# Optimization experiments

Measured on AMD Instinct MI355X. Metric: run time of the kernel, lower is better.

## Reference

```python
import math
import jax, jax.numpy as jnp
import numpy as np

D_MODEL = 256
NUM_HEAD = 8
NUM_LEVEL = 1
KERNEL = 5
NUM_POINT = KERNEL * KERNEL
NUM_VAR = 5  # with_rotation=True
HEAD_DIM = D_MODEL // NUM_HEAD


def _kernel_indices(k=KERNEL):
    # odd kernel: linspace(-(k-1)/2, (k-1)/2, k); torch.meshgrid default 'ij'; stack([j,i])/k
    idx = jnp.linspace(-(k - 1) / 2.0, (k - 1) / 2.0, k)
    ii, jj = jnp.meshgrid(idx, idx, indexing='ij')
    return jnp.stack([jj, ii], axis=-1).reshape(-1, 2) / k  # (P, 2)


def setup_inputs() -> dict:
    key = jax.random.key(0)
    ks = jax.random.split(key, 8)
    B, LQ = 2, 4096
    Hf, Wf = 188, 188
    LV = Hf * Wf
    d = D_MODEL
    nb = NUM_LEVEL * NUM_HEAD * NUM_VAR
    na = NUM_HEAD * NUM_LEVEL * NUM_POINT
    return {
        'query': jax.random.normal(ks[0], (B, LQ, d), jnp.float32),
        'value': jax.random.normal(ks[1], (B, LV, d), jnp.float32),
        'ref_windows': jax.random.uniform(ks[2], (B, LQ, 7), jnp.float32),
        'W_box': jax.random.normal(ks[3], (nb, d), jnp.float32) * 0.02,
        'b_box': jax.random.uniform(ks[4], (nb,), jnp.float32),
        'W_attn': jax.random.normal(ks[5], (na, d), jnp.float32) * 0.02,
        'b_attn': jnp.zeros((na,), jnp.float32),
        'W_value': jax.random.normal(ks[6], (d, d), jnp.float32) * 0.02,
        'b_value': jnp.zeros((d,), jnp.float32),
        'W_out': jax.random.normal(ks[7], (d, d), jnp.float32) * 0.02,
        'b_out': jnp.zeros((d,), jnp.float32),
        'H_feat': Hf,
        'W_feat': Wf,
    }


def reference(query, value, ref_windows, W_box, b_box, W_attn, b_attn,
              W_value, b_value, W_out, b_out, H_feat, W_feat):
    B, LQ, d = query.shape
    LV = value.shape[1]
    Hh, Lv, P, Dh = NUM_HEAD, NUM_LEVEL, NUM_POINT, HEAD_DIM

    # value projection -> (B, LV, Hh, Dh)
    v = (value @ W_value.T + b_value).reshape(B, LV, Hh, Dh)

    # attention weights: softmax over (level*point) per head
    attn = jax.nn.softmax((query @ W_attn.T + b_attn).reshape(B, LQ, Hh, Lv * P), axis=-1)
    attn = attn.reshape(B, LQ, Hh, Lv, P)

    # --- _where_to_attend ---
    ob = (query @ W_box.T + b_box).reshape(B, LQ, Hh, Lv, NUM_VAR)
    rw = ref_windows[:, :, None, None, :]                    # (B,LQ,1,1,7)
    ref_boxes = rw[..., jnp.array([0, 1, 3, 4])]             # cx, cy, w, h
    ref_angles = rw[..., 6:7]
    off_boxes, off_angles = ob[..., :4], ob[..., 4:5]
    angles = (ref_angles + off_angles / 16.0) * (2.0 * math.pi)
    boxes = ref_boxes + off_boxes / 8.0 * ref_boxes[..., jnp.array([2, 3, 2, 3])]
    center = boxes[..., None, :2]                            # (B,LQ,Hh,Lv,1,2)
    size = boxes[..., None, 2:4]
    cos_a, sin_a = jnp.cos(angles), jnp.sin(angles)
    rot = jnp.stack([cos_a, -sin_a, sin_a, cos_a], axis=-1).reshape(B, LQ, Hh, Lv, 1, 2, 2)
    g = _kernel_indices() * jax.nn.relu(size)                # (B,LQ,Hh,Lv,P,2)
    grid = center + (g[..., None, :] * rot).sum(-1)          # (B,LQ,Hh,Lv,P,2), normalized [0,1]

    # --- single-level bilinear sampling (align_corners=False, zero padding) ---
    gl = grid[:, :, :, 0]                                    # (B,LQ,Hh,P,2)
    gx = gl[..., 0] * W_feat - 0.5
    gy = gl[..., 1] * H_feat - 0.5
    x0 = jnp.floor(gx)
    y0 = jnp.floor(gy)
    x0i = x0.astype(jnp.int32)
    y0i = y0.astype(jnp.int32)
    wx1 = gx - x0
    wy1 = gy - y0
    wx0 = 1.0 - wx1
    wy0 = 1.0 - wy1

    b_idx = jnp.arange(B)[:, None, None, None]
    h_idx = jnp.arange(Hh)[None, None, :, None]

    def gather(yi, xi):
        valid = (xi >= 0) & (xi < W_feat) & (yi >= 0) & (yi < H_feat)
        lin = jnp.clip(yi, 0, H_feat - 1) * W_feat + jnp.clip(xi, 0, W_feat - 1)
        return v[b_idx, lin, h_idx] * valid[..., None]       # (B,LQ,Hh,P,Dh)

    s = (gather(y0i, x0i) * (wy0 * wx0)[..., None]
         + gather(y0i, x0i + 1) * (wy0 * wx1)[..., None]
         + gather(y0i + 1, x0i) * (wy1 * wx0)[..., None]
         + gather(y0i + 1, x0i + 1) * (wy1 * wx1)[..., None])

    out_heads = (s * attn[:, :, :, 0, :, None]).sum(axis=3)  # (B,LQ,Hh,Dh)
    out = out_heads.reshape(B, LQ, Hh * Dh) @ W_out.T + b_out
    attn_w = attn.reshape(B, LQ, Hh, Lv, KERNEL, KERNEL)
    return out, attn_w
```

## Files before the change

### kernel.cpp

```cpp
#include <hip/hip_runtime.h>


typedef float floatx4 __attribute__((ext_vector_type(4)));
typedef short shortx8 __attribute__((ext_vector_type(8)));

static __device__ __forceinline__ unsigned short f2bf(float x) {
    unsigned int u = __float_as_uint(x);
    return (unsigned short)((u + 0x7fffu + ((u >> 16) & 1u)) >> 16);
}
static __device__ __forceinline__ unsigned int pack2(float a, float b) {
    return (unsigned int)f2bf(a) | ((unsigned int)f2bf(b) << 16);
}
static __device__ __forceinline__ void async16(const void* g, void* lds) {
    __builtin_amdgcn_global_load_lds(
        (const __attribute__((address_space(1))) unsigned int*)g,
        (__attribute__((address_space(3))) unsigned int*)lds, 16, 0, 0);
}

__global__ __launch_bounds__(256) void convert_kernel(
    const float* __restrict__ value, unsigned short* __restrict__ vbf, long long nv4,
    const float* __restrict__ W_value, unsigned short* __restrict__ wvbf,
    const float* __restrict__ W_attn, const float* __restrict__ W_box,
    unsigned short* __restrict__ wabf, float* __restrict__ Wab,
    const float* __restrict__ W_out, unsigned short* __restrict__ wobf,
    const float* __restrict__ b_attn, const float* __restrict__ b_box,
    float* __restrict__ bab)
{
    const int NBV = 2048;
    const int blk = blockIdx.x, tid = threadIdx.x;
    if (blk < NBV) {
        for (long long i = (long long)blk * 256 + tid; i < nv4; i += (long long)NBV * 256) {
            float4 f = ((const float4*)value)[i];
            ((uint2*)vbf)[i] = make_uint2(pack2(f.x, f.y), pack2(f.z, f.w));
        }
    } else if (blk < NBV + 16) {
        int base = (blk - NBV) * 1024 + tid;
#pragma unroll
        for (int k = 0; k < 4; ++k) {
            int j = base + k * 256;
            float4 f = ((const float4*)W_value)[j];
            ((uint2*)wvbf)[j] = make_uint2(pack2(f.x, f.y), pack2(f.z, f.w));
        }
    } else if (blk < NBV + 32) {
        int base = (blk - NBV - 16) * 1024 + tid;
#pragma unroll
        for (int k = 0; k < 4; ++k) {
            int j = base + k * 256;
            int row = j >> 6, col = (j & 63) * 4;
            float4 f;
            if (row < 200)      f = *(const float4*)(W_attn + (size_t)row * 256 + col);
            else if (row < 240) f = *(const float4*)(W_box + (size_t)(row - 200) * 256 + col);
            else                f = make_float4(0.f, 0.f, 0.f, 0.f);
            ((uint2*)wabf)[j] = make_uint2(pack2(f.x, f.y), pack2(f.z, f.w));
            ((float4*)Wab)[j] = f;
        }
    } else if (blk < NBV + 48) {
        int base = (blk - NBV - 32) * 1024 + tid;
#pragma unroll
        for (int k = 0; k < 4; ++k) {
            int j = base + k * 256;
            float4 f = ((const float4*)W_out)[j];
            ((uint2*)wobf)[j] = make_uint2(pack2(f.x, f.y), pack2(f.z, f.w));
        }
    } else {
        bab[tid] = tid < 200 ? b_attn[tid] : (tid < 240 ? b_box[tid - 200] : 0.f);
    }
}

template <int OUTMODE>
__global__ __launch_bounds__(256) void gemm_bf16(
    const unsigned short* __restrict__ A,
    const unsigned short* __restrict__ Bw,
    const float* __restrict__ bias,
    void* __restrict__ Cv, int M, int LV)
{
    __shared__ unsigned short As[128 * 64];
    __shared__ unsigned short Bs[128 * 64];
    const int tid = threadIdx.x;
    const int wv = tid >> 6, lane = tid & 63;
    const int lr = lane & 15, lq = lane >> 4;
    const int m0 = blockIdx.x * 128, n0 = blockIdx.y * 128;
    const int wm = wv & 1, wn = wv >> 1;
    const int srow = tid >> 3;
    const int scol = (tid & 7) * 8;

    floatx4 acc[4][4];
#pragma unroll
    for (int i = 0; i < 4; ++i)
#pragma unroll
        for (int j = 0; j < 4; ++j) acc[i][j] = (floatx4){0.f, 0.f, 0.f, 0.f};

    for (int kc = 0; kc < 4; ++kc) {
        const int k0 = kc * 64;
        __syncthreads();
#pragma unroll
        for (int i = 0; i < 4; ++i) {
            int ra = m0 + i * 32 + srow; ra = ra < M ? ra : M - 1;
            async16(A + (size_t)ra * 256 + k0 + scol, (char*)As + i * 4096 + wv * 1024);
            int rb = n0 + i * 32 + srow;
            async16(Bw + (size_t)rb * 256 + k0 + scol, (char*)Bs + i * 4096 + wv * 1024);
        }
        __syncthreads();
#pragma unroll
        for (int kk = 0; kk < 64; kk += 32) {
            shortx8 af[4], bfr[4];
#pragma unroll
            for (int t = 0; t < 4; ++t) {
                af[t]  = *(const shortx8*)&As[(wm * 64 + t * 16 + lr) * 64 + kk + lq * 8];
                bfr[t] = *(const shortx8*)&Bs[(wn * 64 + t * 16 + lr) * 64 + kk + lq * 8];
            }
#pragma unroll
            for (int ti = 0; ti < 4; ++ti)
#pragma unroll
                for (int tj = 0; tj < 4; ++tj)
                    acc[ti][tj] = __builtin_amdgcn_mfma_f32_16x16x32_bf16(bfr[tj], af[ti], acc[ti][tj], 0, 0, 0);
        }
    }
#pragma unroll
    for (int ti = 0; ti < 4; ++ti) {
        int m = m0 + wm * 64 + ti * 16 + lr;
        if (m >= M) continue;
        if (OUTMODE == 0) {
            float* Crow = (float*)Cv + (size_t)m * 256;
#pragma unroll
            for (int tj = 0; tj < 4; ++tj) {
                int nb = n0 + wn * 64 + tj * 16 + lq * 4;
                float4 bv = *(const float4*)(bias + nb);
                float4 o = make_float4(acc[ti][tj][0] + bv.x, acc[ti][tj][1] + bv.y,
                                       acc[ti][tj][2] + bv.z, acc[ti][tj][3] + bv.w);
                *(float4*)(Crow + nb) = o;
            }
        } else {
            int b = m >= LV ? 1 : 0;
            int lv = m - (b ? LV : 0);
#pragma unroll
            for (int tj = 0; tj < 4; ++tj) {
                int nb = n0 + wn * 64 + tj * 16 + lq * 4;
                float4 bv = *(const float4*)(bias + nb);
                int h = nb >> 5, dh = nb & 31;
                unsigned short* dst = (unsigned short*)Cv + ((size_t)(b * 8 + h) * LV + lv) * 32 + dh;
                *(uint2*)dst = make_uint2(pack2(acc[ti][tj][0] + bv.x, acc[ti][tj][1] + bv.y),
                                          pack2(acc[ti][tj][2] + bv.z, acc[ti][tj][3] + bv.w));
            }
        }
    }
}

__global__ __launch_bounds__(256) void gemm_nt_bias(
    const float* __restrict__ A, const float* __restrict__ W,
    const float* __restrict__ bias, float* __restrict__ C, int M)
{
    const int K = 256, N = 256;
    __shared__ float As[16][68];
    __shared__ float Bs[16][68];
    int tid = threadIdx.x;
    int tcol = tid & 15, trow = tid >> 4;
    int m0 = blockIdx.x * 64, n0 = blockIdx.y * 64;
    int lr = tid >> 2, lc = (tid & 3) << 2;
    float acc[4][4] = {};
    for (int k0 = 0; k0 < K; k0 += 16) {
        int arow = m0 + lr; if (arow > M - 1) arow = M - 1;
        float4 av = *(const float4*)(A + (size_t)arow * K + k0 + lc);
        float4 wv = *(const float4*)(W + (size_t)(n0 + lr) * K + k0 + lc);
        __syncthreads();
        As[lc + 0][lr] = av.x; As[lc + 1][lr] = av.y; As[lc + 2][lr] = av.z; As[lc + 3][lr] = av.w;
        Bs[lc + 0][lr] = wv.x; Bs[lc + 1][lr] = wv.y; Bs[lc + 2][lr] = wv.z; Bs[lc + 3][lr] = wv.w;
        __syncthreads();
#pragma unroll
        for (int k = 0; k < 16; ++k) {
            float4 a4 = *(const float4*)&As[k][trow << 2];
            float4 b4 = *(const float4*)&Bs[k][tcol << 2];
            float a[4] = {a4.x, a4.y, a4.z, a4.w};
            float bb[4] = {b4.x, b4.y, b4.z, b4.w};
#pragma unroll
            for (int i = 0; i < 4; i++)
#pragma unroll
                for (int j = 0; j < 4; j++) acc[i][j] += a[i] * bb[j];
        }
    }
#pragma unroll
    for (int i = 0; i < 4; i++) {
        int m = m0 + trow * 4 + i;
        if (m >= M) continue;
#pragma unroll
        for (int j = 0; j < 4; j++) {
            int n = n0 + tcol * 4 + j;
            C[(size_t)m * N + n] = acc[i][j] + bias[n];
        }
    }
}

__global__ __launch_bounds__(256) void decode_sample_kernel(
    const unsigned short* __restrict__ v,
    const float* __restrict__ logits,
    const float* __restrict__ ref_windows,
    float* __restrict__ attn_out,
    unsigned short* __restrict__ ohbf,
    const int* __restrict__ Hf_p, const int* __restrict__ Wf_p, int LV, int LQ)
{
    __shared__ float lg[8][32];
    __shared__ float rw[8][7];
    __shared__ float prm[8][6];
    __shared__ float mxinv[8][2];
    __shared__ uint4 pk[8][25][2];

    const int s = blockIdx.x, c = blockIdx.y;
    const int b = s >> 3, h = s & 7;
    const int tid = threadIdx.x;
    const int Hf = *Hf_p, Wf = *Wf_p;
    const size_t mbase = (size_t)b * LQ + c * 8;

    if (tid < 240) {
        int qq = tid / 30, j = tid - qq * 30;
        int col = (j < 25) ? h * 25 + j : 200 + h * 5 + (j - 25);
        lg[qq][j] = logits[(mbase + qq) * 256 + col];
    }
    if (tid < 56) {
        int qq = tid / 7, k = tid - qq * 7;
        rw[qq][k] = ref_windows[(mbase + qq) * 7 + k];
    }
    __syncthreads();

    if (tid < 8) {
        int qq = tid;
        float mx = -1e30f;
#pragma unroll
        for (int p = 0; p < 25; p++) mx = fmaxf(mx, lg[qq][p]);
        float ssum = 0.f;
#pragma unroll
        for (int p = 0; p < 25; p++) ssum += expf(lg[qq][p] - mx);
        mxinv[qq][0] = mx; mxinv[qq][1] = 1.f / ssum;
        float cx = rw[qq][0] + lg[qq][25] * 0.125f * rw[qq][3];
        float cy = rw[qq][1] + lg[qq][26] * 0.125f * rw[qq][4];
        float bw = rw[qq][3] + lg[qq][27] * 0.125f * rw[qq][3];
        float bh = rw[qq][4] + lg[qq][28] * 0.125f * rw[qq][4];
        float ang = (rw[qq][6] + lg[qq][29] * 0.0625f) * 6.283185307179586f;
        prm[qq][0] = cx; prm[qq][1] = cy;
        prm[qq][2] = fmaxf(bw, 0.f); prm[qq][3] = fmaxf(bh, 0.f);
        prm[qq][4] = cosf(ang); prm[qq][5] = sinf(ang);
    }
    __syncthreads();

    if (tid < 200) {
        int qq = tid / 25, p = tid - qq * 25;
        float a = expf(lg[qq][p] - mxinv[qq][0]) * mxinv[qq][1];
        attn_out[(mbase + qq) * 200 + h * 25 + p] = a;
        int pi = p / 5, pj = p - pi * 5;
        float g0 = (float)(pj - 2) * 0.2f * prm[qq][2];
        float g1 = (float)(pi - 2) * 0.2f * prm[qq][3];
        float ca = prm[qq][4], sa = prm[qq][5];
        float gx = (prm[qq][0] + g0 * ca - g1 * sa) * (float)Wf - 0.5f;
        float gy = (prm[qq][1] + g0 * sa + g1 * ca) * (float)Hf - 0.5f;
        float x0f = floorf(gx), y0f = floorf(gy);
        int x0 = (int)x0f, y0 = (int)y0f;
        float wx1 = gx - x0f, wy1 = gy - y0f;
        float wx0 = 1.f - wx1, wy0 = 1.f - wy1;
        int y1 = y0 + 1;
        int bx; float wl, wr;
        if (x0 >= 0 && x0 <= Wf - 2)      { bx = x0;     wl = wx0; wr = wx1; }
        else if (x0 == -1)                { bx = 0;      wl = wx1; wr = 0.f; }
        else if (x0 == Wf - 1)            { bx = Wf - 2; wl = 0.f; wr = wx0; }
        else                              { bx = 0;      wl = 0.f; wr = 0.f; }
        float wy0v = (y0 >= 0 && y0 < Hf) ? wy0 : 0.f;
        float wy1v = (y1 >= 0 && y1 < Hf) ? wy1 : 0.f;
        int cy0 = min(max(y0, 0), Hf - 1), cy1 = min(max(y1, 0), Hf - 1);
        unsigned off0 = (unsigned)(cy0 * Wf + bx) * 16u;
        unsigned off1 = (unsigned)(cy1 * Wf + bx) * 16u;
        float aw0 = a * wy0v, aw1 = a * wy1v;
        pk[qq][p][0] = make_uint4(__float_as_uint(aw0 * wl), __float_as_uint(aw1 * wl), off0, off1);
        pk[qq][p][1] = make_uint4(__float_as_uint(aw0 * wr), __float_as_uint(aw1 * wr), off0, off1);
    }
    __syncthreads();

    const int qq = tid >> 5, l = tid & 31;
    const unsigned int* vw = (const unsigned int*)(v + (size_t)s * LV * 32);
    const uint4* pkp = &pk[qq][0][l >> 4];
    float e0 = 0.f, o0 = 0.f, e1 = 0.f, o1 = 0.f;
#pragma unroll
    for (int p = 0; p < 25; ++p) {
        uint4 t = pkp[2 * p];
        float w0 = __uint_as_float(t.x), w1 = __uint_as_float(t.y);
        unsigned u0 = vw[t.z + l];
        unsigned u1 = vw[t.w + l];
        e0 += w0 * __uint_as_float(u0 << 16);
        o0 += w0 * __uint_as_float(u0 & 0xffff0000u);
        e1 += w1 * __uint_as_float(u1 << 16);
        o1 += w1 * __uint_as_float(u1 & 0xffff0000u);
    }
    float a0 = e0 + e1, a1 = o0 + o1;
    a0 += __shfl_xor(a0, 16, 32);
    a1 += __shfl_xor(a1, 16, 32);
    if (l < 16)
        ((unsigned int*)ohbf)[(mbase + qq) * 128 + h * 16 + l] = pack2(a0, a1);
}

extern "C" void kernel_launch(void* const* d_in, const int* in_sizes, int n_in,
                              void* d_out, int out_size, void* d_ws, size_t ws_size,
                              hipStream_t stream) {
    const float* query       = (const float*)d_in[0];
    const float* value       = (const float*)d_in[1];
    const float* ref_windows = (const float*)d_in[2];
    const float* W_box       = (const float*)d_in[3];
    const float* b_box       = (const float*)d_in[4];
    const float* W_attn      = (const float*)d_in[5];
    const float* b_attn      = (const float*)d_in[6];
    const float* W_value     = (const float*)d_in[7];
    const float* b_value     = (const float*)d_in[8];
    const float* W_out       = (const float*)d_in[9];
    const float* b_out       = (const float*)d_in[10];
    const int*   Hf          = (const int*)d_in[11];
    const int*   Wf          = (const int*)d_in[12];

    const int M1 = in_sizes[1] / 256;
    const int MQ = in_sizes[0] / 256;
    const int LQ = MQ / 2;
    const int LV = M1 / 2;

    unsigned short* vbf  = (unsigned short*)d_ws;
    unsigned short* Vout = vbf + (size_t)M1 * 256;
    unsigned short* ohbf = Vout + (size_t)M1 * 256;
    unsigned short* wvbf = ohbf + (size_t)MQ * 256;
    unsigned short* wabf = wvbf + 65536;
    unsigned short* wobf = wabf + 65536;
    float* Wab       = (float*)(wobf + 65536);
    float* bab       = Wab + 65536;
    float* logits    = bab + 256;

    float* out0     = (float*)d_out;
    float* attn_out = out0 + (size_t)MQ * 256;

    const long long nv4 = (long long)M1 * 64;

    convert_kernel<<<2097, 256, 0, stream>>>(value, vbf, nv4, W_value, wvbf,
                                             W_attn, W_box, wabf, Wab,
                                             W_out, wobf, b_attn, b_box, bab);
    dim3 g1((M1 + 127) / 128, 2);
    gemm_bf16<1><<<g1, 256, 0, stream>>>(vbf, wvbf, b_value, Vout, M1, LV);
    dim3 g2(MQ / 64, 4);
    gemm_nt_bias<<<g2, 256, 0, stream>>>(query, Wab, bab, logits, MQ);
    decode_sample_kernel<<<dim3(16, LQ / 8), 256, 0, stream>>>(
        Vout, logits, ref_windows, attn_out, ohbf, Hf, Wf, LV, LQ);
    dim3 g4(MQ / 128, 2);
    gemm_bf16<0><<<g4, 256, 0, stream>>>(ohbf, wobf, b_out, out0, MQ, LV);
}
```

Baseline: 220.3 us.

## Fuse value fp32-to-bf16 conversion into projection GEMM and retile output GEMM

The separate pass that converted the large value tensor to bf16 is removed. The value-projection GEMM now reads fp32 rows directly, converts them in registers and stores bf16 into shared memory, which avoids a full write and reread of the converted tensor. The output GEMM uses 64-row tiles to launch more blocks, and the decode/sample kernel remaps block indices so consecutive blocks cover the same (batch, head) slices, for better cache locality. The cost is that the fused A loads are synchronous and no longer async-to-LDS, so they may stall the GEMM's load phase.

```diff
diff --git a/kernel.cpp b/kernel.cpp
--- a/kernel.cpp
+++ b/kernel.cpp
@@ -18,31 +18,24 @@
 }
 
 __global__ __launch_bounds__(256) void convert_kernel(
-    const float* __restrict__ value, unsigned short* __restrict__ vbf, long long nv4,
     const float* __restrict__ W_value, unsigned short* __restrict__ wvbf,
     const float* __restrict__ W_attn, const float* __restrict__ W_box,
-    unsigned short* __restrict__ wabf, float* __restrict__ Wab,
+    float* __restrict__ Wab,
     const float* __restrict__ W_out, unsigned short* __restrict__ wobf,
     const float* __restrict__ b_attn, const float* __restrict__ b_box,
     float* __restrict__ bab)
 {
-    const int NBV = 2048;
     const int blk = blockIdx.x, tid = threadIdx.x;
-    if (blk < NBV) {
-        for (long long i = (long long)blk * 256 + tid; i < nv4; i += (long long)NBV * 256) {
-            float4 f = ((const float4*)value)[i];
-            ((uint2*)vbf)[i] = make_uint2(pack2(f.x, f.y), pack2(f.z, f.w));
-        }
-    } else if (blk < NBV + 16) {
-        int base = (blk - NBV) * 1024 + tid;
+    if (blk < 16) {
+        int base = blk * 1024 + tid;
 #pragma unroll
         for (int k = 0; k < 4; ++k) {
             int j = base + k * 256;
             float4 f = ((const float4*)W_value)[j];
             ((uint2*)wvbf)[j] = make_uint2(pack2(f.x, f.y), pack2(f.z, f.w));
         }
-    } else if (blk < NBV + 32) {
-        int base = (blk - NBV - 16) * 1024 + tid;
+    } else if (blk < 32) {
+        int base = (blk - 16) * 1024 + tid;
 #pragma unroll
         for (int k = 0; k < 4; ++k) {
             int j = base + k * 256;
@@ -51,11 +44,10 @@
             if (row < 200)      f = *(const float4*)(W_attn + (size_t)row * 256 + col);
             else if (row < 240) f = *(const float4*)(W_box + (size_t)(row - 200) * 256 + col);
             else                f = make_float4(0.f, 0.f, 0.f, 0.f);
-            ((uint2*)wabf)[j] = make_uint2(pack2(f.x, f.y), pack2(f.z, f.w));
             ((float4*)Wab)[j] = f;
         }
-    } else if (blk < NBV + 48) {
-        int base = (blk - NBV - 32) * 1024 + tid;
+    } else if (blk < 48) {
+        int base = (blk - 32) * 1024 + tid;
 #pragma unroll
         for (int k = 0; k < 4; ++k) {
             int j = base + k * 256;
@@ -67,26 +59,28 @@
     }
 }
 
-template <int OUTMODE>
+template <int OUTMODE, int AFP32, int BM>
 __global__ __launch_bounds__(256) void gemm_bf16(
-    const unsigned short* __restrict__ A,
+    const void* __restrict__ Av,
     const unsigned short* __restrict__ Bw,
     const float* __restrict__ bias,
     void* __restrict__ Cv, int M, int LV)
 {
-    __shared__ unsigned short As[128 * 64];
+    constexpr int NI = BM / 32;
+    constexpr int TI = BM / 32;
+    __shared__ unsigned short As[BM * 64];
     __shared__ unsigned short Bs[128 * 64];
     const int tid = threadIdx.x;
     const int wv = tid >> 6, lane = tid & 63;
     const int lr = lane & 15, lq = lane >> 4;
-    const int m0 = blockIdx.x * 128, n0 = blockIdx.y * 128;
+    const int m0 = blockIdx.x * BM, n0 = blockIdx.y * 128;
     const int wm = wv & 1, wn = wv >> 1;
     const int srow = tid >> 3;
     const int scol = (tid & 7) * 8;
 
-    floatx4 acc[4][4];
-#pragma unroll
-    for (int i = 0; i < 4; ++i)
+    floatx4 acc[TI][4];
+#pragma unroll
+    for (int i = 0; i < TI; ++i)
 #pragma unroll
         for (int j = 0; j < 4; ++j) acc[i][j] = (floatx4){0.f, 0.f, 0.f, 0.f};
 
@@ -95,30 +89,49 @@
         __syncthreads();
 #pragma unroll
         for (int i = 0; i < 4; ++i) {
-            int ra = m0 + i * 32 + srow; ra = ra < M ? ra : M - 1;
-            async16(A + (size_t)ra * 256 + k0 + scol, (char*)As + i * 4096 + wv * 1024);
             int rb = n0 + i * 32 + srow;
             async16(Bw + (size_t)rb * 256 + k0 + scol, (char*)Bs + i * 4096 + wv * 1024);
         }
+        if constexpr (AFP32) {
+            const float* Af = (const float*)Av;
+#pragma unroll
+            for (int i = 0; i < NI; ++i) {
+                int ra = m0 + i * 32 + srow; ra = ra < M ? ra : M - 1;
+                const float* ap = Af + (size_t)ra * 256 + k0 + scol;
+                float4 f0 = *(const float4*)ap;
+                float4 f1 = *(const float4*)(ap + 4);
+                uint4 pv = make_uint4(pack2(f0.x, f0.y), pack2(f0.z, f0.w),
+                                      pack2(f1.x, f1.y), pack2(f1.z, f1.w));
+                *(uint4*)((char*)As + i * 4096 + wv * 1024 + lane * 16) = pv;
+            }
+        } else {
+            const unsigned short* Ab = (const unsigned short*)Av;
+#pragma unroll
+            for (int i = 0; i < NI; ++i) {
+                int ra = m0 + i * 32 + srow; ra = ra < M ? ra : M - 1;
+                async16(Ab + (size_t)ra * 256 + k0 + scol, (char*)As + i * 4096 + wv * 1024);
+            }
+        }
         __syncthreads();
 #pragma unroll
         for (int kk = 0; kk < 64; kk += 32) {
-            shortx8 af[4], bfr[4];
-#pragma unroll
-            for (int t = 0; t < 4; ++t) {
-                af[t]  = *(const shortx8*)&As[(wm * 64 + t * 16 + lr) * 64 + kk + lq * 8];
+            shortx8 af[TI], bfr[4];
+#pragma unroll
+            for (int t = 0; t < TI; ++t)
+                af[t]  = *(const shortx8*)&As[(wm * (BM / 2) + t * 16 + lr) * 64 + kk + lq * 8];
+#pragma unroll
+            for (int t = 0; t < 4; ++t)
                 bfr[t] = *(const shortx8*)&Bs[(wn * 64 + t * 16 + lr) * 64 + kk + lq * 8];
-            }
-#pragma unroll
-            for (int ti = 0; ti < 4; ++ti)
+#pragma unroll
+            for (int ti = 0; ti < TI; ++ti)
 #pragma unroll
                 for (int tj = 0; tj < 4; ++tj)
                     acc[ti][tj] = __builtin_amdgcn_mfma_f32_16x16x32_bf16(bfr[tj], af[ti], acc[ti][tj], 0, 0, 0);
         }
     }
 #pragma unroll
-    for (int ti = 0; ti < 4; ++ti) {
-        int m = m0 + wm * 64 + ti * 16 + lr;
+    for (int ti = 0; ti < TI; ++ti) {
+        int m = m0 + wm * (BM / 2) + ti * 16 + lr;
         if (m >= M) continue;
         if (OUTMODE == 0) {
             float* Crow = (float*)Cv + (size_t)m * 256;
@@ -204,7 +217,11 @@
     __shared__ float mxinv[8][2];
     __shared__ uint4 pk[8][25][2];
 
-    const int s = blockIdx.x, c = blockIdx.y;
+    const int lin = blockIdx.y * 16 + blockIdx.x;
+    const int nc = gridDim.y;
+    const int seq = lin >> 3;
+    const int c = seq % nc;
+    const int s = (lin & 7) + ((seq / nc) << 3);
     const int b = s >> 3, h = s & 7;
     const int tid = threadIdx.x;
     const int Hf = *Hf_p, Wf = *Wf_p;
@@ -316,12 +333,10 @@
     const int LQ = MQ / 2;
     const int LV = M1 / 2;
 
-    unsigned short* vbf  = (unsigned short*)d_ws;
-    unsigned short* Vout = vbf + (size_t)M1 * 256;
+    unsigned short* Vout = (unsigned short*)d_ws;
     unsigned short* ohbf = Vout + (size_t)M1 * 256;
     unsigned short* wvbf = ohbf + (size_t)MQ * 256;
-    unsigned short* wabf = wvbf + 65536;
-    unsigned short* wobf = wabf + 65536;
+    unsigned short* wobf = wvbf + 65536;
     float* Wab       = (float*)(wobf + 65536);
     float* bab       = Wab + 65536;
     float* logits    = bab + 256;
@@ -329,17 +344,14 @@
     float* out0     = (float*)d_out;
     float* attn_out = out0 + (size_t)MQ * 256;
 
-    const long long nv4 = (long long)M1 * 64;
-
-    convert_kernel<<<2097, 256, 0, stream>>>(value, vbf, nv4, W_value, wvbf,
-                                             W_attn, W_box, wabf, Wab,
-                                             W_out, wobf, b_attn, b_box, bab);
+    convert_kernel<<<49, 256, 0, stream>>>(W_value, wvbf, W_attn, W_box, Wab,
+                                           W_out, wobf, b_attn, b_box, bab);
     dim3 g1((M1 + 127) / 128, 2);
-    gemm_bf16<1><<<g1, 256, 0, stream>>>(vbf, wvbf, b_value, Vout, M1, LV);
+    gemm_bf16<1, 1, 128><<<g1, 256, 0, stream>>>(value, wvbf, b_value, Vout, M1, LV);
     dim3 g2(MQ / 64, 4);
     gemm_nt_bias<<<g2, 256, 0, stream>>>(query, Wab, bab, logits, MQ);
     decode_sample_kernel<<<dim3(16, LQ / 8), 256, 0, stream>>>(
         Vout, logits, ref_windows, attn_out, ohbf, Hf, Wf, LV, LQ);
-    dim3 g4(MQ / 128, 2);
-    gemm_bf16<0><<<g4, 256, 0, stream>>>(ohbf, wobf, b_out, out0, MQ, LV);
-}
+    dim3 g4(MQ / 64, 2);
+    gemm_bf16<0, 0, 64><<<g4, 256, 0, stream>>>(ohbf, wobf, b_out, out0, MQ, LV);
+}
```

Result: faster. 215.3 us (-2.3%).
